# Optimization experiments

Measured on AMD Instinct MI355X. Metric: run time of the kernel, lower is better.

The kernel has to match this reference:

```python
import jax, jax.numpy as jnp
import numpy as np

N_HEAD, BS, F_IN, F_OUT = 4, 8192, 64, 64
LEAKY_ALPHA = 0.2


def setup_inputs() -> dict:
    key = jax.random.key(0)
    k1, k2, k3, k4 = jax.random.split(key, 4)
    return {
        "h": jax.random.normal(k1, (BS, F_IN), dtype=jnp.float32),
        "w": jax.random.normal(k2, (N_HEAD, F_IN, F_OUT), dtype=jnp.float32) * (1.0 / np.sqrt(F_IN)),
        "a_src": jax.random.normal(k3, (N_HEAD, F_OUT, 1), dtype=jnp.float32) * (1.0 / np.sqrt(F_OUT)),
        "a_dst": jax.random.normal(k4, (N_HEAD, F_OUT, 1), dtype=jnp.float32) * (1.0 / np.sqrt(F_OUT)),
        "bias": jnp.zeros((F_OUT,), dtype=jnp.float32),
    }


def reference(h, w, a_src, a_dst, bias):
    # h: [bs, f_in] broadcast-matmul with w: [n_head, f_in, f_out] -> [n_head, bs, f_out]
    h_prime = jnp.einsum("bi,hio->hbo", h, w)
    attn_src = jnp.einsum("hbo,ho->hb", h_prime, a_src[..., 0])  # [n_head, bs]
    attn_dst = jnp.einsum("hbo,ho->hb", h_prime, a_dst[..., 0])  # [n_head, bs]
    # additive scores: [n_head, bs, bs]
    attn = attn_src[:, :, None] + attn_dst[:, None, :]
    attn = jnp.where(attn >= 0, attn, LEAKY_ALPHA * attn)  # leaky_relu(0.2)
    attn = jax.nn.softmax(attn, axis=-1)
    # dropout is identity at inference
    out = jnp.einsum("hbn,hno->hbo", attn, h_prime) + bias  # [n_head, bs, f_out]
    out = jnp.transpose(out, (1, 0, 2))  # [bs, n_head, f_out]
    return out.reshape(out.shape[0], -1)  # [bs, n_head*f_out]
```

## Files before the change

kernel.cpp:

```cpp
#include <hip/hip_runtime.h>
#include <stdio.h>

#define H 4
#define B 8192
#define F 64
#define ALPHA 0.2f
#define NB 4096
#define DMIN (-8.0f)
#define DSCALE 256.0f
#define TSZ 16
#define NTL (B / TSZ)
#define PELD 132

__device__ __forceinline__ int bucket_of(float x)
{
  int b = (int)((x - DMIN) * DSCALE);
  return min(max(b, 0), NB - 1);
}

__global__ __launch_bounds__(256) void k_hprime(
    const float* __restrict__ h, const float* __restrict__ w,
    const float* __restrict__ a_src, const float* __restrict__ a_dst,
    float* __restrict__ hp, float* __restrict__ s, float* __restrict__ d)
{
  int head = blockIdx.y;
  int row0 = blockIdx.x * 64;
  __shared__ float wl[F * F];
  __shared__ float hl[64 * F];
  const float4* wsrc = (const float4*)(w + (size_t)head * F * F);
  const float4* hsrc = (const float4*)(h + (size_t)row0 * F);
  float4* wl4 = (float4*)wl;
  float4* hl4 = (float4*)hl;
  for (int t = threadIdx.x; t < F * F / 4; t += 256) { wl4[t] = wsrc[t]; hl4[t] = hsrc[t]; }
  __syncthreads();
  int o  = threadIdx.x & 63;
  int rb = threadIdx.x >> 6;
  float as = a_src[head * F + o];
  float ad = a_dst[head * F + o];
  float acc[16];
#pragma unroll
  for (int rg = 0; rg < 16; ++rg) acc[rg] = 0.f;
#pragma unroll 4
  for (int i4 = 0; i4 < F / 4; ++i4) {
    float w0 = wl[(4 * i4 + 0) * F + o];
    float w1 = wl[(4 * i4 + 1) * F + o];
    float w2 = wl[(4 * i4 + 2) * F + o];
    float w3 = wl[(4 * i4 + 3) * F + o];
#pragma unroll
    for (int rg = 0; rg < 16; ++rg) {
      float4 h4 = *((const float4*)(hl + (rg * 4 + rb) * F) + i4);
      acc[rg] = fmaf(h4.x, w0, fmaf(h4.y, w1, fmaf(h4.z, w2, fmaf(h4.w, w3, acc[rg]))));
    }
  }
#pragma unroll
  for (int rg = 0; rg < 16; ++rg) {
    int r = row0 + rg * 4 + rb;
    hp[((size_t)head * B + r) * F + o] = acc[rg];
    float vs = acc[rg] * as, vd = acc[rg] * ad;
#pragma unroll
    for (int off = 32; off; off >>= 1) { vs += __shfl_down(vs, off); vd += __shfl_down(vd, off); }
    if (o == 0) {
      s[(size_t)head * B + r] = vs;
      d[(size_t)head * B + r] = vd;
    }
  }
}

__global__ __launch_bounds__(1024) void k_hist_scan(
    const float* __restrict__ d, int* __restrict__ bstart, int* __restrict__ gcur)
{
  int head = blockIdx.x;
  int tid = threadIdx.x;
  __shared__ int hist[NB];
  __shared__ int wtot[16], woff[16];
#pragma unroll
  for (int t = 0; t < NB / 1024; ++t) hist[tid + t * 1024] = 0;
  __syncthreads();
  const float* dh = d + (size_t)head * B;
#pragma unroll
  for (int t = 0; t < B / 1024; ++t)
    atomicAdd(&hist[bucket_of(dh[tid + t * 1024])], 1);
  __syncthreads();
  int h0 = hist[4 * tid], h1 = hist[4 * tid + 1], h2 = hist[4 * tid + 2], h3 = hist[4 * tid + 3];
  int sum = h0 + h1 + h2 + h3;
  int lane = tid & 63, wid = tid >> 6;
  int run = sum;
#pragma unroll
  for (int off = 1; off < 64; off <<= 1) {
    int v = __shfl_up(run, off);
    if (lane >= off) run += v;
  }
  if (lane == 63) wtot[wid] = run;
  __syncthreads();
  if (tid < 16) {
    int off = 0;
    for (int j = 0; j < tid; ++j) off += wtot[j];
    woff[tid] = off;
  }
  __syncthreads();
  int excl = woff[wid] + run - sum;
  int base = head * (NB + 1) + 4 * tid;
  int gbase = head * NB + 4 * tid;
  int e0 = excl, e1 = e0 + h0, e2 = e1 + h1, e3 = e2 + h2;
  bstart[base] = e0; bstart[base + 1] = e1; bstart[base + 2] = e2; bstart[base + 3] = e3;
  gcur[gbase] = e0; gcur[gbase + 1] = e1; gcur[gbase + 2] = e2; gcur[gbase + 3] = e3;
  if (tid == 1023) bstart[head * (NB + 1) + NB] = e3 + h3;
}

__global__ __launch_bounds__(512) void k_scatter(
    const float* __restrict__ d, int* __restrict__ gcur,
    float* __restrict__ ds, int* __restrict__ is)
{
  int head = blockIdx.y;
  int i = blockIdx.x * 512 + threadIdx.x;
  float v = d[(size_t)head * B + i];
  int b = bucket_of(v);
  int pos = atomicAdd(&gcur[head * NB + b], 1);
  ds[(size_t)head * B + pos] = v;
  is[(size_t)head * B + pos] = i;
}

__global__ __launch_bounds__(256) void k_sort(
    const float* __restrict__ dsort, const int* __restrict__ isort,
    const int* __restrict__ bstart, float* __restrict__ ds2, int* __restrict__ js2)
{
  int head = blockIdx.y;
  int b = blockIdx.x * 4 + (threadIdx.x >> 6);
  int lane = threadIdx.x & 63;
  int k0 = bstart[head * (NB + 1) + b];
  int k1 = bstart[head * (NB + 1) + b + 1];
  const float* dh = dsort + (size_t)head * B;
  const int*   ih = isort + (size_t)head * B;
  for (int e = k0 + lane; e < k1; e += 64) {
    float dv = dh[e]; int iv = ih[e];
    int rank = 0;
    for (int k = k0; k < k1; ++k) {
      float d2 = dh[k]; int i2 = ih[k];
      rank += (d2 < dv) || (d2 == dv && i2 < iv);
    }
    ds2[(size_t)head * B + k0 + rank] = dv;
    js2[(size_t)head * B + k0 + rank] = iv;
  }
}

__global__ __launch_bounds__(256) void k_peA(
    const float* __restrict__ ds2, const int* __restrict__ js2,
    const float* __restrict__ hp, float* __restrict__ TS)
{
  int head = blockIdx.y;
  int tile = blockIdx.x * 4 + (threadIdx.x >> 6);
  int o = threadIdx.x & 63;
  int k0 = tile * TSZ;
  const float* dsh = ds2 + (size_t)head * B;
  const int*   jsh = js2 + (size_t)head * B;
  const float* hph = hp + (size_t)head * B * F;
  float e1[TSZ], e2[TSZ], hv[TSZ];
  int jj[TSZ];
#pragma unroll
  for (int j = 0; j < TSZ; ++j) jj[j] = jsh[k0 + j];
#pragma unroll
  for (int j = 0; j < TSZ; ++j) hv[j] = hph[(size_t)jj[j] * F + o];
#pragma unroll
  for (int j = 0; j < TSZ; ++j) {
    float dv = dsh[k0 + j];
    e1[j] = expf(dv); e2[j] = expf(ALPHA * dv);
  }
  float a1 = 0.f, a2 = 0.f, s1 = 0.f, s2 = 0.f;
#pragma unroll
  for (int j = 0; j < TSZ; ++j) {
    a1 = fmaf(e1[j], hv[j], a1);
    a2 = fmaf(e2[j], hv[j], a2);
    s1 += e1[j]; s2 += e2[j];
  }
  float* row = TS + ((size_t)head * NTL + tile) * PELD;
  row[o] = a1; row[64 + o] = a2;
  if (o == 0) { row[128] = s1; row[129] = s2; }
}

__global__ __launch_bounds__(64) void k_peB(
    float* __restrict__ TS, float* __restrict__ totals)
{
  int head = blockIdx.y;
  int c = blockIdx.x;
  int lane = threadIdx.x;
  float* base = TS + (size_t)head * NTL * PELD + c;
  int t0 = lane * 8;
  float v[8];
#pragma unroll
  for (int t = 0; t < 8; ++t) v[t] = base[(size_t)(t0 + t) * PELD];
  float sum = 0.f;
#pragma unroll
  for (int t = 0; t < 8; ++t) { sum += v[t]; v[t] = sum; }
  float run = sum;
#pragma unroll
  for (int off = 1; off < 64; off <<= 1) {
    float u = __shfl_up(run, off);
    if (lane >= off) run += u;
  }
  float excl = run - sum;
  if (lane == 63) totals[head * PELD + c] = run;
#pragma unroll
  for (int t = 0; t < 8; ++t)
    base[(size_t)(t0 + t) * PELD] = excl + (t == 0 ? 0.f : v[t - 1]);
}

__global__ __launch_bounds__(256) void k_peC(
    const float* __restrict__ ds2, const int* __restrict__ js2,
    const float* __restrict__ hp, const float* __restrict__ TS,
    float* __restrict__ PE)
{
  int head = blockIdx.y;
  int tile = blockIdx.x * 4 + (threadIdx.x >> 6);
  int o = threadIdx.x & 63;
  int k0 = tile * TSZ;
  const float* dsh = ds2 + (size_t)head * B;
  const int*   jsh = js2 + (size_t)head * B;
  const float* hph = hp + (size_t)head * B * F;
  float e1[TSZ], e2[TSZ], hv[TSZ];
  int jj[TSZ];
#pragma unroll
  for (int j = 0; j < TSZ; ++j) jj[j] = jsh[k0 + j];
#pragma unroll
  for (int j = 0; j < TSZ; ++j) hv[j] = hph[(size_t)jj[j] * F + o];
#pragma unroll
  for (int j = 0; j < TSZ; ++j) {
    float dv = dsh[k0 + j];
    e1[j] = expf(dv); e2[j] = expf(ALPHA * dv);
  }
  const float* trow = TS + ((size_t)head * NTL + tile) * PELD;
  float a1 = trow[o], a2 = trow[64 + o], s1 = trow[128], s2 = trow[129];
#pragma unroll
  for (int j = 0; j < TSZ; ++j) {
    float* row = PE + ((size_t)head * B + k0 + j) * PELD;
    row[o] = a1; row[64 + o] = a2;
    if (o == 0) { row[128] = s1; row[129] = s2; }
    a1 = fmaf(e1[j], hv[j], a1);
    a2 = fmaf(e2[j], hv[j], a2);
    s1 += e1[j]; s2 += e2[j];
  }
}

__global__ __launch_bounds__(256) void k_out(
    const float* __restrict__ s, const float* __restrict__ ds2,
    const float* __restrict__ PE, const float* __restrict__ totals,
    const int* __restrict__ bstart, const float* __restrict__ bias,
    float* __restrict__ out)
{
  int head = blockIdx.y;
  int i = blockIdx.x * 4 + (threadIdx.x >> 6);
  int o = threadIdx.x & 63;
  float si = s[(size_t)head * B + i];
  float t = -si;
  int q = bucket_of(t);
  int k  = bstart[head * (NB + 1) + q];
  int Eq = bstart[head * (NB + 1) + q + 1];
  const float* dsh = ds2 + (size_t)head * B;
  while (k < Eq && dsh[k] < t) ++k;
  const float* row = (k < B) ? (PE + ((size_t)head * B + k) * PELD)
                             : (totals + head * PELD);
  float pe1 = row[o], pe2 = row[64 + o], p1 = row[128], p2 = row[129];
  float TE1 = totals[head * PELD + o];
  float T1  = totals[head * PELD + 128];
  float e1f = expf(si), e2f = expf(ALPHA * si);
  float denom = e2f * p2 + e1f * (T1 - p1);
  float num   = e2f * pe2 + e1f * (TE1 - pe1);
  out[(size_t)i * (H * F) + head * F + o] = num / denom + bias[o];
}

extern "C" void kernel_launch(void* const* d_in, const int* in_sizes, int n_in,
                              void* d_out, int out_size, void* d_ws, size_t ws_size,
                              hipStream_t stream)
{
  const float* h     = (const float*)d_in[0];
  const float* w     = (const float*)d_in[1];
  const float* a_src = (const float*)d_in[2];
  const float* a_dst = (const float*)d_in[3];
  const float* bias  = (const float*)d_in[4];
  float* out = (float*)d_out;

  float* p = (float*)d_ws;
  float* hp     = p; p += (size_t)H * B * F;
  float* s      = p; p += H * B;
  float* dd     = p; p += H * B;
  float* dsort  = p; p += H * B;
  int*   isort  = (int*)p; p += H * B;
  float* ds2    = p; p += H * B;
  int*   js2    = (int*)p; p += H * B;
  float* PE     = p; p += (size_t)H * B * PELD;
  float* TS     = p; p += (size_t)H * NTL * PELD;
  float* totals = p; p += H * PELD;
  int* bstart   = (int*)p; p += H * (NB + 1);
  int* gcur     = (int*)p; p += H * NB;

  size_t need = (size_t)((char*)p - (char*)d_ws);
  if (ws_size < need) {
    fprintf(stderr, "kernel_launch: ws_size %zu < needed %zu\n", ws_size, need);
    return;
  }

  k_hprime<<<dim3(B / 64, H), 256, 0, stream>>>(h, w, a_src, a_dst, hp, s, dd);
  k_hist_scan<<<H, 1024, 0, stream>>>(dd, bstart, gcur);
  k_scatter<<<dim3(B / 512, H), 512, 0, stream>>>(dd, gcur, dsort, isort);
  k_sort<<<dim3(NB / 4, H), 256, 0, stream>>>(dsort, isort, bstart, ds2, js2);
  k_peA<<<dim3(NTL / 4, H), 256, 0, stream>>>(ds2, js2, hp, TS);
  k_peB<<<dim3(130, H), 64, 0, stream>>>(TS, totals);
  k_peC<<<dim3(NTL / 4, H), 256, 0, stream>>>(ds2, js2, hp, TS, PE);
  k_out<<<dim3(B / 4, H), 256, 0, stream>>>(s, ds2, PE, totals, bstart, bias, out);
}
```

Baseline: 74.81 us.

## Merge queries into sort stream and fuse prefix expansion with output

Query keys (-s) are now sorted together with the key values d into one merged stream of length 2B. The materialized per-position prefix array PE and the separate output kernel with its bucket search go away. Each tile walks the merged sequence and emits outputs for the queries it meets, using the running prefix sums. This removes a large PE write and read plus the binary-search pass, at the cost of doubling the sort, scatter and tile scan work and making output writes scattered.

```diff
diff --git a/kernel.cpp b/kernel.cpp
--- a/kernel.cpp
+++ b/kernel.cpp
@@ -3,13 +3,14 @@
 
 #define H 4
 #define B 8192
+#define M2 (2 * B)
 #define F 64
 #define ALPHA 0.2f
 #define NB 4096
 #define DMIN (-8.0f)
 #define DSCALE 256.0f
 #define TSZ 16
-#define NTL (B / TSZ)
+#define NTL2 (M2 / TSZ)
 #define PELD 132
 
 __device__ __forceinline__ int bucket_of(float x)
@@ -67,7 +68,8 @@
 }
 
 __global__ __launch_bounds__(1024) void k_hist_scan(
-    const float* __restrict__ d, int* __restrict__ bstart, int* __restrict__ gcur)
+    const float* __restrict__ s, const float* __restrict__ d,
+    int* __restrict__ bstart, int* __restrict__ gcur)
 {
   int head = blockIdx.x;
   int tid = threadIdx.x;
@@ -76,7 +78,11 @@
 #pragma unroll
   for (int t = 0; t < NB / 1024; ++t) hist[tid + t * 1024] = 0;
   __syncthreads();
+  const float* sh = s + (size_t)head * B;
   const float* dh = d + (size_t)head * B;
+#pragma unroll
+  for (int t = 0; t < B / 1024; ++t)
+    atomicAdd(&hist[bucket_of(-sh[tid + t * 1024])], 1);
 #pragma unroll
   for (int t = 0; t < B / 1024; ++t)
     atomicAdd(&hist[bucket_of(dh[tid + t * 1024])], 1);
@@ -108,62 +114,63 @@
 }
 
 __global__ __launch_bounds__(512) void k_scatter(
-    const float* __restrict__ d, int* __restrict__ gcur,
-    float* __restrict__ ds, int* __restrict__ is)
-{
-  int head = blockIdx.y;
-  int i = blockIdx.x * 512 + threadIdx.x;
-  float v = d[(size_t)head * B + i];
+    const float* __restrict__ s, const float* __restrict__ d, int* __restrict__ gcur,
+    float* __restrict__ vsort, int* __restrict__ gsort)
+{
+  int head = blockIdx.y;
+  int g = blockIdx.x * 512 + threadIdx.x;
+  float v = (g < B) ? -s[(size_t)head * B + g] : d[(size_t)head * B + (g - B)];
   int b = bucket_of(v);
   int pos = atomicAdd(&gcur[head * NB + b], 1);
-  ds[(size_t)head * B + pos] = v;
-  is[(size_t)head * B + pos] = i;
+  vsort[(size_t)head * M2 + pos] = v;
+  gsort[(size_t)head * M2 + pos] = g;
 }
 
 __global__ __launch_bounds__(256) void k_sort(
-    const float* __restrict__ dsort, const int* __restrict__ isort,
-    const int* __restrict__ bstart, float* __restrict__ ds2, int* __restrict__ js2)
+    const float* __restrict__ vsort, const int* __restrict__ gsort,
+    const int* __restrict__ bstart, float* __restrict__ vs2, int* __restrict__ gs2)
 {
   int head = blockIdx.y;
   int b = blockIdx.x * 4 + (threadIdx.x >> 6);
   int lane = threadIdx.x & 63;
   int k0 = bstart[head * (NB + 1) + b];
   int k1 = bstart[head * (NB + 1) + b + 1];
-  const float* dh = dsort + (size_t)head * B;
-  const int*   ih = isort + (size_t)head * B;
+  const float* vh = vsort + (size_t)head * M2;
+  const int*   gh = gsort + (size_t)head * M2;
   for (int e = k0 + lane; e < k1; e += 64) {
-    float dv = dh[e]; int iv = ih[e];
+    float vv = vh[e]; int gv = gh[e];
     int rank = 0;
     for (int k = k0; k < k1; ++k) {
-      float d2 = dh[k]; int i2 = ih[k];
-      rank += (d2 < dv) || (d2 == dv && i2 < iv);
-    }
-    ds2[(size_t)head * B + k0 + rank] = dv;
-    js2[(size_t)head * B + k0 + rank] = iv;
+      float v2 = vh[k]; int g2 = gh[k];
+      rank += (v2 < vv) || (v2 == vv && g2 < gv);
+    }
+    vs2[(size_t)head * M2 + k0 + rank] = vv;
+    gs2[(size_t)head * M2 + k0 + rank] = gv;
   }
 }
 
 __global__ __launch_bounds__(256) void k_peA(
-    const float* __restrict__ ds2, const int* __restrict__ js2,
+    const float* __restrict__ vs2, const int* __restrict__ gs2,
     const float* __restrict__ hp, float* __restrict__ TS)
 {
   int head = blockIdx.y;
   int tile = blockIdx.x * 4 + (threadIdx.x >> 6);
   int o = threadIdx.x & 63;
   int k0 = tile * TSZ;
-  const float* dsh = ds2 + (size_t)head * B;
-  const int*   jsh = js2 + (size_t)head * B;
+  const float* vsh = vs2 + (size_t)head * M2;
+  const int*   gsh = gs2 + (size_t)head * M2;
   const float* hph = hp + (size_t)head * B * F;
-  float e1[TSZ], e2[TSZ], hv[TSZ];
-  int jj[TSZ];
-#pragma unroll
-  for (int j = 0; j < TSZ; ++j) jj[j] = jsh[k0 + j];
-#pragma unroll
-  for (int j = 0; j < TSZ; ++j) hv[j] = hph[(size_t)jj[j] * F + o];
-#pragma unroll
-  for (int j = 0; j < TSZ; ++j) {
-    float dv = dsh[k0 + j];
-    e1[j] = expf(dv); e2[j] = expf(ALPHA * dv);
+  float vv[TSZ]; int gg[TSZ];
+#pragma unroll
+  for (int j = 0; j < TSZ; ++j) { vv[j] = vsh[k0 + j]; gg[j] = gsh[k0 + j]; }
+  float hv[TSZ], e1[TSZ], e2[TSZ];
+#pragma unroll
+  for (int j = 0; j < TSZ; ++j)
+    hv[j] = (gg[j] >= B) ? hph[(size_t)(gg[j] - B) * F + o] : 0.f;
+#pragma unroll
+  for (int j = 0; j < TSZ; ++j) {
+    e1[j] = (gg[j] >= B) ? expf(vv[j]) : 0.f;
+    e2[j] = (gg[j] >= B) ? expf(ALPHA * vv[j]) : 0.f;
   }
   float a1 = 0.f, a2 = 0.f, s1 = 0.f, s2 = 0.f;
 #pragma unroll
@@ -172,7 +179,7 @@
     a2 = fmaf(e2[j], hv[j], a2);
     s1 += e1[j]; s2 += e2[j];
   }
-  float* row = TS + ((size_t)head * NTL + tile) * PELD;
+  float* row = TS + ((size_t)head * NTL2 + tile) * PELD;
   row[o] = a1; row[64 + o] = a2;
   if (o == 0) { row[128] = s1; row[129] = s2; }
 }
@@ -183,14 +190,14 @@
   int head = blockIdx.y;
   int c = blockIdx.x;
   int lane = threadIdx.x;
-  float* base = TS + (size_t)head * NTL * PELD + c;
-  int t0 = lane * 8;
-  float v[8];
-#pragma unroll
-  for (int t = 0; t < 8; ++t) v[t] = base[(size_t)(t0 + t) * PELD];
+  float* base = TS + (size_t)head * NTL2 * PELD + c;
+  int t0 = lane * 16;
+  float v[16];
+#pragma unroll
+  for (int t = 0; t < 16; ++t) v[t] = base[(size_t)(t0 + t) * PELD];
   float sum = 0.f;
 #pragma unroll
-  for (int t = 0; t < 8; ++t) { sum += v[t]; v[t] = sum; }
+  for (int t = 0; t < 16; ++t) { sum += v[t]; v[t] = sum; }
   float run = sum;
 #pragma unroll
   for (int off = 1; off < 64; off <<= 1) {
@@ -200,71 +207,55 @@
   float excl = run - sum;
   if (lane == 63) totals[head * PELD + c] = run;
 #pragma unroll
-  for (int t = 0; t < 8; ++t)
+  for (int t = 0; t < 16; ++t)
     base[(size_t)(t0 + t) * PELD] = excl + (t == 0 ? 0.f : v[t - 1]);
 }
 
-__global__ __launch_bounds__(256) void k_peC(
-    const float* __restrict__ ds2, const int* __restrict__ js2,
+__global__ __launch_bounds__(256) void k_peC_out(
+    const float* __restrict__ vs2, const int* __restrict__ gs2,
     const float* __restrict__ hp, const float* __restrict__ TS,
-    float* __restrict__ PE)
+    const float* __restrict__ totals, const float* __restrict__ bias,
+    float* __restrict__ out)
 {
   int head = blockIdx.y;
   int tile = blockIdx.x * 4 + (threadIdx.x >> 6);
   int o = threadIdx.x & 63;
   int k0 = tile * TSZ;
-  const float* dsh = ds2 + (size_t)head * B;
-  const int*   jsh = js2 + (size_t)head * B;
+  const float* vsh = vs2 + (size_t)head * M2;
+  const int*   gsh = gs2 + (size_t)head * M2;
   const float* hph = hp + (size_t)head * B * F;
-  float e1[TSZ], e2[TSZ], hv[TSZ];
-  int jj[TSZ];
-#pragma unroll
-  for (int j = 0; j < TSZ; ++j) jj[j] = jsh[k0 + j];
-#pragma unroll
-  for (int j = 0; j < TSZ; ++j) hv[j] = hph[(size_t)jj[j] * F + o];
-#pragma unroll
-  for (int j = 0; j < TSZ; ++j) {
-    float dv = dsh[k0 + j];
-    e1[j] = expf(dv); e2[j] = expf(ALPHA * dv);
-  }
-  const float* trow = TS + ((size_t)head * NTL + tile) * PELD;
+  float vv[TSZ]; int gg[TSZ];
+#pragma unroll
+  for (int j = 0; j < TSZ; ++j) { vv[j] = vsh[k0 + j]; gg[j] = gsh[k0 + j]; }
+  float hv[TSZ], e1[TSZ], e2[TSZ];
+#pragma unroll
+  for (int j = 0; j < TSZ; ++j)
+    hv[j] = (gg[j] >= B) ? hph[(size_t)(gg[j] - B) * F + o] : 0.f;
+#pragma unroll
+  for (int j = 0; j < TSZ; ++j) {
+    e1[j] = (gg[j] >= B) ? expf(vv[j]) : 0.f;
+    e2[j] = (gg[j] >= B) ? expf(ALPHA * vv[j]) : 0.f;
+  }
+  const float* trow = TS + ((size_t)head * NTL2 + tile) * PELD;
   float a1 = trow[o], a2 = trow[64 + o], s1 = trow[128], s2 = trow[129];
-#pragma unroll
-  for (int j = 0; j < TSZ; ++j) {
-    float* row = PE + ((size_t)head * B + k0 + j) * PELD;
-    row[o] = a1; row[64 + o] = a2;
-    if (o == 0) { row[128] = s1; row[129] = s2; }
-    a1 = fmaf(e1[j], hv[j], a1);
-    a2 = fmaf(e2[j], hv[j], a2);
-    s1 += e1[j]; s2 += e2[j];
-  }
-}
-
-__global__ __launch_bounds__(256) void k_out(
-    const float* __restrict__ s, const float* __restrict__ ds2,
-    const float* __restrict__ PE, const float* __restrict__ totals,
-    const int* __restrict__ bstart, const float* __restrict__ bias,
-    float* __restrict__ out)
-{
-  int head = blockIdx.y;
-  int i = blockIdx.x * 4 + (threadIdx.x >> 6);
-  int o = threadIdx.x & 63;
-  float si = s[(size_t)head * B + i];
-  float t = -si;
-  int q = bucket_of(t);
-  int k  = bstart[head * (NB + 1) + q];
-  int Eq = bstart[head * (NB + 1) + q + 1];
-  const float* dsh = ds2 + (size_t)head * B;
-  while (k < Eq && dsh[k] < t) ++k;
-  const float* row = (k < B) ? (PE + ((size_t)head * B + k) * PELD)
-                             : (totals + head * PELD);
-  float pe1 = row[o], pe2 = row[64 + o], p1 = row[128], p2 = row[129];
   float TE1 = totals[head * PELD + o];
   float T1  = totals[head * PELD + 128];
-  float e1f = expf(si), e2f = expf(ALPHA * si);
-  float denom = e2f * p2 + e1f * (T1 - p1);
-  float num   = e2f * pe2 + e1f * (TE1 - pe1);
-  out[(size_t)i * (H * F) + head * F + o] = num / denom + bias[o];
+  float bo  = bias[o];
+#pragma unroll
+  for (int j = 0; j < TSZ; ++j) {
+    if (gg[j] < B) {
+      int i = gg[j];
+      float si = -vv[j];
+      float e1f = expf(si), e2f = expf(ALPHA * si);
+      float denom = e2f * s2 + e1f * (T1 - s1);
+      float num   = e2f * a2 + e1f * (TE1 - a1);
+      out[(size_t)i * (H * F) + head * F + o] = num / denom + bo;
+    } else {
+      a1 = fmaf(e1[j], hv[j], a1);
+      a2 = fmaf(e2[j], hv[j], a2);
+      s1 += e1[j]; s2 += e2[j];
+    }
+  }
 }
 
 extern "C" void kernel_launch(void* const* d_in, const int* in_sizes, int n_in,
@@ -282,12 +273,11 @@
   float* hp     = p; p += (size_t)H * B * F;
   float* s      = p; p += H * B;
   float* dd     = p; p += H * B;
-  float* dsort  = p; p += H * B;
-  int*   isort  = (int*)p; p += H * B;
-  float* ds2    = p; p += H * B;
-  int*   js2    = (int*)p; p += H * B;
-  float* PE     = p; p += (size_t)H * B * PELD;
-  float* TS     = p; p += (size_t)H * NTL * PELD;
+  float* vsort  = p; p += (size_t)H * M2;
+  int*   gsort  = (int*)p; p += (size_t)H * M2;
+  float* vs2    = p; p += (size_t)H * M2;
+  int*   gs2    = (int*)p; p += (size_t)H * M2;
+  float* TS     = p; p += (size_t)H * NTL2 * PELD;
   float* totals = p; p += H * PELD;
   int* bstart   = (int*)p; p += H * (NB + 1);
   int* gcur     = (int*)p; p += H * NB;
@@ -299,11 +289,10 @@
   }
 
   k_hprime<<<dim3(B / 64, H), 256, 0, stream>>>(h, w, a_src, a_dst, hp, s, dd);
-  k_hist_scan<<<H, 1024, 0, stream>>>(dd, bstart, gcur);
-  k_scatter<<<dim3(B / 512, H), 512, 0, stream>>>(dd, gcur, dsort, isort);
-  k_sort<<<dim3(NB / 4, H), 256, 0, stream>>>(dsort, isort, bstart, ds2, js2);
-  k_peA<<<dim3(NTL / 4, H), 256, 0, stream>>>(ds2, js2, hp, TS);
+  k_hist_scan<<<H, 1024, 0, stream>>>(s, dd, bstart, gcur);
+  k_scatter<<<dim3(M2 / 512, H), 512, 0, stream>>>(s, dd, gcur, vsort, gsort);
+  k_sort<<<dim3(NB / 4, H), 256, 0, stream>>>(vsort, gsort, bstart, vs2, gs2);
+  k_peA<<<dim3(NTL2 / 4, H), 256, 0, stream>>>(vs2, gs2, hp, TS);
   k_peB<<<dim3(130, H), 64, 0, stream>>>(TS, totals);
-  k_peC<<<dim3(NTL / 4, H), 256, 0, stream>>>(ds2, js2, hp, TS, PE);
-  k_out<<<dim3(B / 4, H), 256, 0, stream>>>(s, ds2, PE, totals, bstart, bias, out);
-}
+  k_peC_out<<<dim3(NTL2 / 4, H), 256, 0, stream>>>(vs2, gs2, hp, TS, totals, bias, out);
+}
```

Measured after the change: 75.61 us. Within noise of the previous version (+1.1%).
